# Optimization experiments

Measured on AMD Instinct MI355X. Metric: run time of the kernel, lower is better.

The kernel has to match this reference:

```python
import jax, jax.numpy as jnp
import numpy as np

D_MODEL = 256   # per-head dim in this module
N_HEAD = 8
B, S = 4, 2048
NEG_INF = -1e9  # large negative in place of -inf for numerical safety


def setup_inputs() -> dict:
    key = jax.random.key(0)
    ks = jax.random.split(key, 8)
    d, h = D_MODEL, N_HEAD
    sc = 1.0 / np.sqrt(d)
    return {
        "Q": jax.random.normal(ks[0], (B, S, d), jnp.float32),
        "mask": jax.random.randint(ks[1], (B, S), 0, 2, jnp.int32),
        "WQ_w": jax.random.normal(ks[2], (h * d, d), jnp.float32) * sc,
        "WQ_b": jnp.zeros((h * d,), jnp.float32),
        "WK_w": jax.random.normal(ks[3], (h * d, d), jnp.float32) * sc,
        "WK_b": jnp.zeros((h * d,), jnp.float32),
        "WV_w": jax.random.normal(ks[4], (h * d, d), jnp.float32) * sc,
        "WV_b": jnp.zeros((h * d,), jnp.float32),
        "WO_w": jax.random.normal(ks[5], (d, h * d), jnp.float32) * sc,
        "WO_b": jnp.zeros((d,), jnp.float32),
        "ln_g": jnp.ones((d,), jnp.float32),
        "ln_b": jnp.zeros((d,), jnp.float32),
    }


def reference(Q, mask, WQ_w, WQ_b, WK_w, WK_b, WV_w, WV_b, WO_w, WO_b, ln_g, ln_b):
    b, s, d = Q.shape
    h = N_HEAD
    # projections (torch Linear: x @ W.T + b), split into heads: [b, h, s, d]
    q = (Q @ WQ_w.T + WQ_b).reshape(b, s, h, d).transpose(0, 2, 1, 3)
    k = (Q @ WK_w.T + WK_b).reshape(b, s, h, d).transpose(0, 2, 1, 3)
    v = (Q @ WV_w.T + WV_b).reshape(b, s, h, d).transpose(0, 2, 1, 3)
    # scaled dot-product scores [b, h, q, k]
    scores = jnp.einsum('bhqd,bhkd->bhqk', q, k) / jnp.sqrt(jnp.asarray(d, Q.dtype))
    key_mask = (mask != 0)[:, None, None, :]  # [b,1,1,k]
    scores = jnp.where(key_mask, scores, NEG_INF)
    alpha = jax.nn.softmax(scores, axis=-1)
    out = jnp.einsum('bhqk,bhkd->bhqd', alpha, v)
    out = out.transpose(0, 2, 1, 3).reshape(b, s, h * d)
    out = out @ WO_w.T + WO_b + Q  # dropout is identity in eval
    # LayerNorm over last dim
    mu = out.mean(-1, keepdims=True)
    var = out.var(-1, keepdims=True)
    return (out - mu) / jnp.sqrt(var + 1e-5) * ln_g + ln_b
```

## Files before the change

kernel.cpp:

```cpp
#include <hip/hip_runtime.h>
#include <cstddef>
#include <cstdint>

#define SQ 2048
#define DH 256
#define NH 8
#define BATCH 4
#define MROWS (BATCH*SQ)
#define HID (NH*DH)

typedef __attribute__((ext_vector_type(8)))  short bf16x8;
typedef __attribute__((ext_vector_type(16))) float f32x16;

typedef __attribute__((address_space(1))) const unsigned char gbuf_t;
typedef __attribute__((address_space(3))) unsigned char lbuf_t;

__device__ __forceinline__ void gl_lds16(const void* g, void* l) {
  __builtin_amdgcn_global_load_lds((gbuf_t*)g, (lbuf_t*)l, 16, 0, 0);
}

__device__ __forceinline__ unsigned short f2bf(float f) {
  unsigned u = __float_as_uint(f);
  unsigned r = (u + 0x7FFFu + ((u >> 16) & 1u)) >> 16;
  return (unsigned short)r;
}
__device__ __forceinline__ unsigned pk2(float a, float b) {
  return (unsigned)f2bf(a) | ((unsigned)f2bf(b) << 16);
}
__device__ __forceinline__ f32x16 zero16() {
  f32x16 v;
#pragma unroll
  for (int i = 0; i < 16; ++i) v[i] = 0.0f;
  return v;
}

__global__ void __launch_bounds__(256) cvt_kernel(
    const float* __restrict__ X,  const float* __restrict__ Wq,
    const float* __restrict__ Wk, const float* __restrict__ Wv,
    const float* __restrict__ Wo,
    unsigned short* __restrict__ Xb,  unsigned short* __restrict__ Wqb,
    unsigned short* __restrict__ Wkb, unsigned short* __restrict__ Wvb,
    unsigned short* __restrict__ Wob)
{
  int bid = blockIdx.x;
  const float* src; unsigned short* dst; size_t off;
  if      (bid < 512) { src = X;  dst = Xb;  off = (size_t)bid * 4096; }
  else if (bid < 640) { src = Wq; dst = Wqb; off = (size_t)(bid - 512) * 4096; }
  else if (bid < 768) { src = Wk; dst = Wkb; off = (size_t)(bid - 640) * 4096; }
  else if (bid < 896) { src = Wv; dst = Wvb; off = (size_t)(bid - 768) * 4096; }
  else                { src = Wo; dst = Wob; off = (size_t)(bid - 896) * 4096; }
  int tid = threadIdx.x;
#pragma unroll
  for (int k = 0; k < 4; ++k) {
    size_t idx = off + ((size_t)k * 256 + tid) * 4;
    float4 v = *(const float4*)(src + idx);
    uint2 o; o.x = pk2(v.x, v.y); o.y = pk2(v.z, v.w);
    *(uint2*)(dst + idx) = o;
  }
}

__global__ void __launch_bounds__(256) qkv_kernel(
    const unsigned short* __restrict__ Xbf,
    const unsigned short* __restrict__ Wqb,
    const unsigned short* __restrict__ Wkb,
    const unsigned short* __restrict__ Wvb,
    const float* __restrict__ bq, const float* __restrict__ bk, const float* __restrict__ bv,
    unsigned short* __restrict__ q_ws, unsigned short* __restrict__ k_ws,
    unsigned short* __restrict__ vt_ws)
{
  __shared__ unsigned char TA[65536];
  __shared__ unsigned char TB[65536];
  const int tid = threadIdx.x, w = tid >> 6, l = tid & 63;
  const int h = l >> 5, t = l & 31;
  const int wm = w >> 1, wn = w & 1;
  const int z = blockIdx.z;
  const int m0 = (z == 2) ? blockIdx.y * 128 : blockIdx.x * 128;
  const int n0 = (z == 2) ? blockIdx.x * 128 : blockIdx.y * 128;
  const unsigned short* Asrc = (z == 2) ? Wvb : Xbf;
  const unsigned short* Bsrc = (z == 0) ? Wqb : (z == 1) ? Wkb : Xbf;

  const int rowo = l >> 5;
  const int bin  = (l & 31) * 16;
#pragma unroll
  for (int i2 = 0; i2 < 16; ++i2) {
    int i = 16 * w + i2;
    int row = 2 * i + rowo;
    gl_lds16((const unsigned char*)(Asrc + (size_t)(m0 + row) * 256) + (bin ^ ((row & 15) << 4)),
             &TA[i * 1024]);
  }
#pragma unroll
  for (int i2 = 0; i2 < 16; ++i2) {
    int i = 16 * w + i2;
    int row = 2 * i + rowo;
    gl_lds16((const unsigned char*)(Bsrc + (size_t)(n0 + row) * 256) + (bin ^ ((row & 15) << 4)),
             &TB[i * 1024]);
  }
  __syncthreads();

  f32x16 acc00 = zero16(), acc01 = zero16(), acc10 = zero16(), acc11 = zero16();
  const int swz = (t & 15) << 4;
#pragma unroll
  for (int kc = 0; kc < 16; ++kc) {
    int kb = (32 * kc + 16 * h) ^ swz;
    bf16x8 a0 = *(const bf16x8*)&TA[(size_t)(64 * wm + t) * 512 + kb];
    bf16x8 a1 = *(const bf16x8*)&TA[(size_t)(64 * wm + 32 + t) * 512 + kb];
    bf16x8 b0 = *(const bf16x8*)&TB[(size_t)(64 * wn + t) * 512 + kb];
    bf16x8 b1 = *(const bf16x8*)&TB[(size_t)(64 * wn + 32 + t) * 512 + kb];
    acc00 = __builtin_amdgcn_mfma_f32_32x32x16_bf16(a0, b0, acc00, 0, 0, 0);
    acc01 = __builtin_amdgcn_mfma_f32_32x32x16_bf16(a0, b1, acc01, 0, 0, 0);
    acc10 = __builtin_amdgcn_mfma_f32_32x32x16_bf16(a1, b0, acc10, 0, 0, 0);
    acc11 = __builtin_amdgcn_mfma_f32_32x32x16_bf16(a1, b1, acc11, 0, 0, 0);
  }

  if (z < 2) {
    unsigned short* outp = z ? k_ws : q_ws;
    const float* bias = z ? bk : bq;
    float bn0 = bias[n0 + 64 * wn + t];
    float bn1 = bias[n0 + 64 * wn + 32 + t];
#pragma unroll
    for (int mt = 0; mt < 2; ++mt) {
#pragma unroll
      for (int nt = 0; nt < 2; ++nt) {
        int n = n0 + 64 * wn + 32 * nt + t;
        int headn = n >> 8, d = n & 255;
        float bb = nt ? bn1 : bn0;
        const f32x16& A = (mt == 0) ? (nt == 0 ? acc00 : acc01) : (nt == 0 ? acc10 : acc11);
#pragma unroll
        for (int r = 0; r < 16; ++r) {
          int m = m0 + 64 * wm + 32 * mt + (r & 3) + 8 * (r >> 2) + 4 * h;
          int batch = m >> 11, s = m & 2047;
          outp[(((size_t)batch * NH + headn) * SQ + s) * DH + d] = f2bf(A[r] + bb);
        }
      }
    }
  } else {
#pragma unroll
    for (int mt = 0; mt < 2; ++mt) {
#pragma unroll
      for (int r = 0; r < 16; ++r) {
        int j = m0 + 64 * wm + 32 * mt + (r & 3) + 8 * (r >> 2) + 4 * h;
        float bj = bv[j];
        int headj = j >> 8, jl = j & 255;
#pragma unroll
        for (int nt = 0; nt < 2; ++nt) {
          int sall = n0 + 64 * wn + 32 * nt + t;
          int batch = sall >> 11, ss = sall & 2047;
          const f32x16& A = (mt == 0) ? (nt == 0 ? acc00 : acc01) : (nt == 0 ? acc10 : acc11);
          vt_ws[((size_t)batch * NH + headj) * DH * SQ + (size_t)jl * SQ + ss] = f2bf(A[r] + bj);
        }
      }
    }
  }
}

__global__ void __launch_bounds__(256, 2) attn_kernel(
    const unsigned short* __restrict__ q_ws,
    const unsigned short* __restrict__ k_ws,
    const unsigned short* __restrict__ vt_ws,
    const int* __restrict__ mask,
    unsigned short* __restrict__ o_ws)
{
  __shared__ unsigned char KT[32768];
  __shared__ unsigned char VT[32768];
  __shared__ float MB[2048];

  const int tid = threadIdx.x, w = tid >> 6, l = tid & 63;
  const int h = l >> 5, t = l & 31;
  const int bh = blockIdx.y;
  const int b = bh >> 3, head = bh & 7;
  const int q0 = blockIdx.x * 128;

  {
    const int* mrow = mask + b * SQ;
    for (int i = tid; i < SQ; i += 256) MB[i] = mrow[i] ? 0.0f : -1e9f;
  }

  bf16x8 qf[16];
  {
    const unsigned short* qb = q_ws + ((size_t)bh * SQ + (q0 + 32 * w + t)) * DH + 8 * h;
#pragma unroll
    for (int kc = 0; kc < 16; ++kc) qf[kc] = *(const bf16x8*)(qb + 16 * kc);
  }

  f32x16 o[8];
#pragma unroll
  for (int i = 0; i < 8; ++i) o[i] = zero16();
  float m_run = -3.0e38f, l_run = 0.0f;

  const int swzK = (t & 15) << 4;
  const int swzV = (t & 7) << 4;
  const int krow_off = l >> 5, kb_in = (l & 31) * 16;
  const int vrow_off = l >> 3, vb_in = (l & 7) * 16;
  const unsigned short* kplane = k_ws + (size_t)bh * SQ * DH;
  const unsigned short* vplane = vt_ws + (size_t)bh * DH * SQ;

  for (int kb = 0; kb < SQ; kb += 64) {
    __syncthreads();
#pragma unroll
    for (int i2 = 0; i2 < 8; ++i2) {
      int i = 8 * w + i2;
      int row = 2 * i + krow_off;
      gl_lds16((const unsigned char*)(kplane + (size_t)(kb + row) * DH) + (kb_in ^ ((row & 15) << 4)),
               &KT[i * 1024]);
    }
#pragma unroll
    for (int i2 = 0; i2 < 8; ++i2) {
      int i = 8 * w + i2;
      int row = 8 * i + vrow_off;
      gl_lds16((const unsigned char*)(vplane + (size_t)row * SQ + kb) + (vb_in ^ ((row & 7) << 4)),
               &VT[i * 1024]);
    }
    __syncthreads();

    f32x16 sa0 = zero16(), sa1 = zero16();
#pragma unroll
    for (int kc = 0; kc < 16; ++kc) {
      int kbb = (32 * kc + 16 * h) ^ swzK;
      bf16x8 a0 = *(const bf16x8*)&KT[(size_t)t * 512 + kbb];
      bf16x8 a1 = *(const bf16x8*)&KT[(size_t)(32 + t) * 512 + kbb];
      sa0 = __builtin_amdgcn_mfma_f32_32x32x16_bf16(a0, qf[kc], sa0, 0, 0, 0);
      sa1 = __builtin_amdgcn_mfma_f32_32x32x16_bf16(a1, qf[kc], sa1, 0, 0, 0);
    }

    float tm = -3.0e38f;
    const float* mbp = &MB[kb + 4 * h];
#pragma unroll
    for (int r = 0; r < 16; ++r) {
      int kl = (r & 3) + 8 * (r >> 2);
      sa0[r] = sa0[r] * 0.0625f + mbp[kl];
      sa1[r] = sa1[r] * 0.0625f + mbp[32 + kl];
      tm = fmaxf(tm, fmaxf(sa0[r], sa1[r]));
    }
    tm = fmaxf(tm, __shfl_xor(tm, 32, 64));
    float m_new = fmaxf(m_run, tm);
    float rf = __expf(m_run - m_new);
    m_run = m_new;
    float ls = 0.0f;
#pragma unroll
    for (int r = 0; r < 16; ++r) {
      sa0[r] = __expf(sa0[r] - m_new);
      sa1[r] = __expf(sa1[r] - m_new);
      ls += sa0[r] + sa1[r];
    }
    ls += __shfl_xor(ls, 32, 64);
    l_run = l_run * rf + ls;

#pragma unroll
    for (int r = 0; r < 16; ++r) {
      float rr = __shfl(rf, (r & 3) + 8 * (r >> 2) + 4 * h, 64);
#pragma unroll
      for (int db = 0; db < 8; ++db) o[db][r] *= rr;
    }

    bf16x8 pa[4];
#pragma unroll
    for (int ks = 0; ks < 4; ++ks) {
      const f32x16& P = (ks < 2) ? sa0 : sa1;
      const int base = 8 * (ks & 1);
      unsigned lo0 = pk2(P[base + 0], P[base + 1]);
      unsigned lo1 = pk2(P[base + 2], P[base + 3]);
      unsigned hi0 = pk2(P[base + 4], P[base + 5]);
      unsigned hi1 = pk2(P[base + 6], P[base + 7]);
      unsigned s0 = h ? lo0 : hi0;
      unsigned s1 = h ? lo1 : hi1;
      unsigned x0 = (unsigned)__shfl_xor((int)s0, 32, 64);
      unsigned x1 = (unsigned)__shfl_xor((int)s1, 32, 64);
      union { unsigned u[4]; bf16x8 v; } pu;
      pu.u[0] = h ? x0 : lo0;
      pu.u[1] = h ? x1 : lo1;
      pu.u[2] = h ? hi0 : x0;
      pu.u[3] = h ? hi1 : x1;
      pa[ks] = pu.v;
    }

#pragma unroll
    for (int db = 0; db < 8; ++db) {
#pragma unroll
      for (int ks = 0; ks < 4; ++ks) {
        bf16x8 bv = *(const bf16x8*)&VT[(size_t)(32 * db + t) * 128 + ((32 * ks + 16 * h) ^ swzV)];
        o[db] = __builtin_amdgcn_mfma_f32_32x32x16_bf16(pa[ks], bv, o[db], 0, 0, 0);
      }
    }
  }

  float linv = 1.0f / l_run;
  unsigned short* ob = o_ws + (size_t)b * SQ * HID + (size_t)head * DH;
#pragma unroll
  for (int r = 0; r < 16; ++r) {
    int rowr = (r & 3) + 8 * (r >> 2) + 4 * h;
    float li = __shfl(linv, rowr, 64);
    int s = q0 + 32 * w + rowr;
    unsigned short* orow = ob + (size_t)s * HID;
#pragma unroll
    for (int db = 0; db < 8; ++db)
      orow[32 * db + t] = f2bf(o[db][r] * li);
  }
}

__global__ void __launch_bounds__(256) oproj_kernel(
    const unsigned short* __restrict__ Abf,
    const unsigned short* __restrict__ Wob,
    float* __restrict__ tmp)
{
  __shared__ unsigned char TA[8192];
  __shared__ unsigned char TB[16384];
  const int tid = threadIdx.x, w = tid >> 6, l = tid & 63;
  const int h = l >> 5, t = l & 31;
  const int wm = w >> 1, wn = w & 1;
  const int m0 = blockIdx.x * 64, n0 = blockIdx.y * 128;
  const int arow_o = l >> 3, ab_in = (l & 7) * 16;
  const int swz = (t & 7) << 4;

  f32x16 acc0 = zero16(), acc1 = zero16();
  for (int chunk = 0; chunk < 32; ++chunk) {
    __syncthreads();
#pragma unroll
    for (int i2 = 0; i2 < 2; ++i2) {
      int i = 2 * w + i2;
      int row = 8 * i + arow_o;
      gl_lds16((const unsigned char*)(Abf + (size_t)(m0 + row) * HID + chunk * 64) + (ab_in ^ ((row & 7) << 4)),
               &TA[i * 1024]);
    }
#pragma unroll
    for (int i2 = 0; i2 < 4; ++i2) {
      int i = 4 * w + i2;
      int row = 8 * i + arow_o;
      gl_lds16((const unsigned char*)(Wob + (size_t)(n0 + row) * HID + chunk * 64) + (ab_in ^ ((row & 7) << 4)),
               &TB[i * 1024]);
    }
    __syncthreads();
#pragma unroll
    for (int kc = 0; kc < 4; ++kc) {
      int kbb = (32 * kc + 16 * h) ^ swz;
      bf16x8 a  = *(const bf16x8*)&TA[(size_t)(32 * wm + t) * 128 + kbb];
      bf16x8 b0 = *(const bf16x8*)&TB[(size_t)(64 * wn + t) * 128 + kbb];
      bf16x8 b1 = *(const bf16x8*)&TB[(size_t)(64 * wn + 32 + t) * 128 + kbb];
      acc0 = __builtin_amdgcn_mfma_f32_32x32x16_bf16(a, b0, acc0, 0, 0, 0);
      acc1 = __builtin_amdgcn_mfma_f32_32x32x16_bf16(a, b1, acc1, 0, 0, 0);
    }
  }
#pragma unroll
  for (int nt = 0; nt < 2; ++nt) {
    const f32x16& A = nt ? acc1 : acc0;
    int n = n0 + 64 * wn + 32 * nt + t;
#pragma unroll
    for (int r = 0; r < 16; ++r) {
      int m = m0 + 32 * wm + (r & 3) + 8 * (r >> 2) + 4 * h;
      tmp[(size_t)m * DH + n] = A[r];
    }
  }
}

__global__ void __launch_bounds__(256) ln_kernel(
    const float* __restrict__ tmp, const float* __restrict__ bo,
    const float* __restrict__ Xin, const float* __restrict__ g,
    const float* __restrict__ be, float* __restrict__ out)
{
  const int tid = threadIdx.x, w = tid >> 6, lane = tid & 63;
  const int row = blockIdx.x * 4 + w;
  float4 v  = ((const float4*)(tmp + (size_t)row * DH))[lane];
  float4 qv = ((const float4*)(Xin + (size_t)row * DH))[lane];
  float4 bb = ((const float4*)bo)[lane];
  v.x += qv.x + bb.x; v.y += qv.y + bb.y; v.z += qv.z + bb.z; v.w += qv.w + bb.w;
  float s1 = v.x + v.y + v.z + v.w;
  float s2 = v.x * v.x + v.y * v.y + v.z * v.z + v.w * v.w;
#pragma unroll
  for (int off = 1; off < 64; off <<= 1) {
    s1 += __shfl_xor(s1, off, 64);
    s2 += __shfl_xor(s2, off, 64);
  }
  float mean = s1 * (1.0f / 256.0f);
  float var = s2 * (1.0f / 256.0f) - mean * mean;
  float rstd = rsqrtf(var + 1e-5f);
  float4 gg = ((const float4*)g)[lane];
  float4 b2 = ((const float4*)be)[lane];
  float4 o;
  o.x = (v.x - mean) * rstd * gg.x + b2.x;
  o.y = (v.y - mean) * rstd * gg.y + b2.y;
  o.z = (v.z - mean) * rstd * gg.z + b2.z;
  o.w = (v.w - mean) * rstd * gg.w + b2.w;
  ((float4*)(out + (size_t)row * DH))[lane] = o;
}

extern "C" void kernel_launch(void* const* d_in, const int* in_sizes, int n_in,
                              void* d_out, int out_size, void* d_ws, size_t ws_size,
                              hipStream_t stream) {
  const float* Q    = (const float*)d_in[0];
  const int*   mask = (const int*)  d_in[1];
  const float* WQ_w = (const float*)d_in[2];
  const float* WQ_b = (const float*)d_in[3];
  const float* WK_w = (const float*)d_in[4];
  const float* WK_b = (const float*)d_in[5];
  const float* WV_w = (const float*)d_in[6];
  const float* WV_b = (const float*)d_in[7];
  const float* WO_w = (const float*)d_in[8];
  const float* WO_b = (const float*)d_in[9];
  const float* ln_g = (const float*)d_in[10];
  const float* ln_b = (const float*)d_in[11];
  float* out = (float*)d_out;

  uint8_t* ws = (uint8_t*)d_ws;
  const size_t MB1 = 1048576;
  unsigned short* Xb   = (unsigned short*)(ws + 0 * MB1);
  unsigned short* Wqb  = (unsigned short*)(ws + 4 * MB1);
  unsigned short* Wkb  = (unsigned short*)(ws + 5 * MB1);
  unsigned short* Wvb  = (unsigned short*)(ws + 6 * MB1);
  unsigned short* Wob  = (unsigned short*)(ws + 7 * MB1);
  unsigned short* q_ws = (unsigned short*)(ws + 8 * MB1);
  unsigned short* k_ws = (unsigned short*)(ws + 40 * MB1);
  unsigned short* vtws = (unsigned short*)(ws + 72 * MB1);
  unsigned short* o_ws = (unsigned short*)(ws + 104 * MB1);
  float*          tmpf = (float*)         (ws + 136 * MB1);

  cvt_kernel<<<1024, 256, 0, stream>>>(Q, WQ_w, WK_w, WV_w, WO_w, Xb, Wqb, Wkb, Wvb, Wob);
  qkv_kernel<<<dim3(64, 16, 3), 256, 0, stream>>>(Xb, Wqb, Wkb, Wvb, WQ_b, WK_b, WV_b,
                                                  q_ws, k_ws, vtws);
  attn_kernel<<<dim3(16, 32), 256, 0, stream>>>(q_ws, k_ws, vtws, mask, o_ws);
  oproj_kernel<<<dim3(128, 2), 256, 0, stream>>>(o_ws, Wob, tmpf);
  ln_kernel<<<2048, 256, 0, stream>>>(tmpf, WO_b, Q, ln_g, ln_b, out);
}
```

Measured before the change: 354.8 us.

## Double-buffer K/V tiles in attention with 512-thread blocks and XCD-aware mapping

```diff
diff --git a/kernel.cpp b/kernel.cpp
--- a/kernel.cpp
+++ b/kernel.cpp
@@ -153,27 +153,33 @@
   }
 }
 
-__global__ void __launch_bounds__(256, 2) attn_kernel(
+__global__ void __launch_bounds__(512, 2) attn_kernel(
     const unsigned short* __restrict__ q_ws,
     const unsigned short* __restrict__ k_ws,
     const unsigned short* __restrict__ vt_ws,
     const int* __restrict__ mask,
     unsigned short* __restrict__ o_ws)
 {
-  __shared__ unsigned char KT[32768];
-  __shared__ unsigned char VT[32768];
+  __shared__ unsigned char KT[2][32768];
+  __shared__ unsigned char VT[2][32768];
   __shared__ float MB[2048];
 
   const int tid = threadIdx.x, w = tid >> 6, l = tid & 63;
   const int h = l >> 5, t = l & 31;
-  const int bh = blockIdx.y;
+  const int bid = blockIdx.x;
+  const int xcd = bid & 7, slot = bid >> 3;
+  const int bh = xcd * 4 + (slot >> 3);
+  const int qt = slot & 7;
   const int b = bh >> 3, head = bh & 7;
-  const int q0 = blockIdx.x * 128;
+  const int q0 = qt * 256;
 
   {
     const int* mrow = mask + b * SQ;
-    for (int i = tid; i < SQ; i += 256) MB[i] = mrow[i] ? 0.0f : -1e9f;
-  }
+    for (int i = tid; i < SQ; i += 512) MB[i] = mrow[i] ? 0.0f : -1e9f;
+  }
+
+  const unsigned short* kplane = k_ws + (size_t)bh * SQ * DH;
+  const unsigned short* vplane = vt_ws + (size_t)bh * DH * SQ;
 
   bf16x8 qf[16];
   {
@@ -182,6 +188,27 @@
     for (int kc = 0; kc < 16; ++kc) qf[kc] = *(const bf16x8*)(qb + 16 * kc);
   }
 
+  const int krow_o = l >> 5, kcol = (l & 31) * 16;
+  const int vrow_o = l >> 3, vcol = (l & 7) * 16;
+
+  {
+#pragma unroll
+    for (int i = 0; i < 4; ++i) {
+      int j = 4 * w + i;
+      int row = 2 * j + krow_o;
+      gl_lds16((const unsigned char*)(kplane + (size_t)row * DH) + (kcol ^ ((row & 15) << 4)),
+               &KT[0][j * 1024]);
+    }
+#pragma unroll
+    for (int i = 0; i < 4; ++i) {
+      int j = 4 * w + i;
+      int row = 8 * j + vrow_o;
+      gl_lds16((const unsigned char*)(vplane + (size_t)row * SQ) + (vcol ^ ((row & 7) << 4)),
+               &VT[0][j * 1024]);
+    }
+  }
+  __syncthreads();
+
   f32x16 o[8];
 #pragma unroll
   for (int i = 0; i < 8; ++i) o[i] = zero16();
@@ -189,38 +216,38 @@
 
   const int swzK = (t & 15) << 4;
   const int swzV = (t & 7) << 4;
-  const int krow_off = l >> 5, kb_in = (l & 31) * 16;
-  const int vrow_off = l >> 3, vb_in = (l & 7) * 16;
-  const unsigned short* kplane = k_ws + (size_t)bh * SQ * DH;
-  const unsigned short* vplane = vt_ws + (size_t)bh * DH * SQ;
-
+
+  int cur = 0;
   for (int kb = 0; kb < SQ; kb += 64) {
-    __syncthreads();
-#pragma unroll
-    for (int i2 = 0; i2 < 8; ++i2) {
-      int i = 8 * w + i2;
-      int row = 2 * i + krow_off;
-      gl_lds16((const unsigned char*)(kplane + (size_t)(kb + row) * DH) + (kb_in ^ ((row & 15) << 4)),
-               &KT[i * 1024]);
-    }
-#pragma unroll
-    for (int i2 = 0; i2 < 8; ++i2) {
-      int i = 8 * w + i2;
-      int row = 8 * i + vrow_off;
-      gl_lds16((const unsigned char*)(vplane + (size_t)row * SQ + kb) + (vb_in ^ ((row & 7) << 4)),
-               &VT[i * 1024]);
-    }
-    __syncthreads();
+    const int nxt = cur ^ 1;
+    if (kb + 64 < SQ) {
+#pragma unroll
+      for (int i = 0; i < 4; ++i) {
+        int j = 4 * w + i;
+        int row = 2 * j + krow_o;
+        gl_lds16((const unsigned char*)(kplane + (size_t)(kb + 64 + row) * DH) + (kcol ^ ((row & 15) << 4)),
+                 &KT[nxt][j * 1024]);
+      }
+#pragma unroll
+      for (int i = 0; i < 4; ++i) {
+        int j = 4 * w + i;
+        int row = 8 * j + vrow_o;
+        gl_lds16((const unsigned char*)(vplane + (size_t)row * SQ + kb + 64) + (vcol ^ ((row & 7) << 4)),
+                 &VT[nxt][j * 1024]);
+      }
+    }
 
     f32x16 sa0 = zero16(), sa1 = zero16();
+    __builtin_amdgcn_s_setprio(1);
 #pragma unroll
     for (int kc = 0; kc < 16; ++kc) {
       int kbb = (32 * kc + 16 * h) ^ swzK;
-      bf16x8 a0 = *(const bf16x8*)&KT[(size_t)t * 512 + kbb];
-      bf16x8 a1 = *(const bf16x8*)&KT[(size_t)(32 + t) * 512 + kbb];
+      bf16x8 a0 = *(const bf16x8*)&KT[cur][(size_t)t * 512 + kbb];
+      bf16x8 a1 = *(const bf16x8*)&KT[cur][(size_t)(32 + t) * 512 + kbb];
       sa0 = __builtin_amdgcn_mfma_f32_32x32x16_bf16(a0, qf[kc], sa0, 0, 0, 0);
       sa1 = __builtin_amdgcn_mfma_f32_32x32x16_bf16(a1, qf[kc], sa1, 0, 0, 0);
     }
+    __builtin_amdgcn_s_setprio(0);
 
     float tm = -3.0e38f;
     const float* mbp = &MB[kb + 4 * h];
@@ -273,14 +300,19 @@
       pa[ks] = pu.v;
     }
 
+    __builtin_amdgcn_s_setprio(1);
 #pragma unroll
     for (int db = 0; db < 8; ++db) {
 #pragma unroll
       for (int ks = 0; ks < 4; ++ks) {
-        bf16x8 bv = *(const bf16x8*)&VT[(size_t)(32 * db + t) * 128 + ((32 * ks + 16 * h) ^ swzV)];
+        bf16x8 bv = *(const bf16x8*)&VT[cur][(size_t)(32 * db + t) * 128 + ((32 * ks + 16 * h) ^ swzV)];
         o[db] = __builtin_amdgcn_mfma_f32_32x32x16_bf16(pa[ks], bv, o[db], 0, 0, 0);
       }
     }
+    __builtin_amdgcn_s_setprio(0);
+
+    __syncthreads();
+    cur = nxt;
   }
 
   float linv = 1.0f / l_run;
@@ -415,7 +447,7 @@
   cvt_kernel<<<1024, 256, 0, stream>>>(Q, WQ_w, WK_w, WV_w, WO_w, Xb, Wqb, Wkb, Wvb, Wob);
   qkv_kernel<<<dim3(64, 16, 3), 256, 0, stream>>>(Xb, Wqb, Wkb, Wvb, WQ_b, WK_b, WV_b,
                                                   q_ws, k_ws, vtws);
-  attn_kernel<<<dim3(16, 32), 256, 0, stream>>>(q_ws, k_ws, vtws, mask, o_ws);
+  attn_kernel<<<dim3(256), 512, 0, stream>>>(q_ws, k_ws, vtws, mask, o_ws);
   oproj_kernel<<<dim3(128, 2), 256, 0, stream>>>(o_ws, Wob, tmpf);
   ln_kernel<<<2048, 256, 0, stream>>>(tmpf, WO_b, Q, ln_g, ln_b, out);
 }
```

Result: faster. 312.0 us (-12.0%).
